# Kernel tuning notes

Hardware: AMD Instinct MI355X
Metric: run time of the kernel (lower is better)

Reference implementation:

```python
import jax, jax.numpy as jnp
import numpy as np

BATCH = 256
MAX_STEP = 200
NUM_Q = 1000


def setup_inputs() -> dict:
    key = jax.random.key(0)
    k1, k2 = jax.random.split(key)
    # predictions strictly inside (0, 1) for BCE
    pred = jax.random.uniform(k1, (BATCH, MAX_STEP - 1, NUM_Q), dtype=jnp.float32) * 0.98 + 0.01
    # sparse binary error-ID labels; some rows all-zero -> masked out (ragged structure)
    batch = (jax.random.uniform(k2, (BATCH, MAX_STEP, NUM_Q)) < 0.002).astype(jnp.float32)
    # guarantee every student has at least one attempted row (torch BCE on empty -> NaN)
    batch = batch.at[:, 1, 0].set(1.0)
    return {"pred": pred, "batch": batch}


def reference(pred, batch):
    # ErrorIDs path: gt = batch[student][1:], keep rows containing any 1.
    gt = batch[:, 1:, :]                              # [B, T-1, Q]
    row_mask = jnp.any(gt == 1.0, axis=-1)            # [B, T-1] ragged mask
    m = row_mask[:, :, None].astype(pred.dtype)       # [B, T-1, 1]

    # nn.BCELoss: -(y*log(p) + (1-y)*log(1-p)), logs clamped at -100, mean reduction
    log_p = jnp.maximum(jnp.log(pred), -100.0)
    log_1mp = jnp.maximum(jnp.log1p(-pred), -100.0)
    bce = -(gt * log_p + (1.0 - gt) * log_1mp)        # [B, T-1, Q]

    n_elem = row_mask.sum(axis=1).astype(pred.dtype) * gt.shape[-1]  # selected elements per student
    per_student = (bce * m).sum(axis=(1, 2)) / n_elem               # mean BCE per student
    loss = per_student.sum()                                        # summed over students

    # Original returns ragged concatenations of selected rows; we return the
    # equivalent masked full tensors plus the row mask (same information, jit-friendly).
    return (loss, pred * m, gt * m, row_mask)
```

## Files before the change

### kernel.cpp

```cpp
#include <hip/hip_runtime.h>

#define BATCHN 256
#define TSTEPS 199
#define NQ     1000
#define NROWS  (BATCHN * TSTEPS)
#define RPB    4
#define NBLOCKS (NROWS / RPB)

__global__ void zero_ws_kernel(float* __restrict__ ws) {
    int i = threadIdx.x;
    if (i < 2 * BATCHN) ws[i] = 0.0f;
}

typedef float f4v __attribute__((ext_vector_type(4)));

__device__ __forceinline__ f4v loadu4(const float* p) {
    f4v v; __builtin_memcpy(&v, p, 16); return v;
}

__global__ __launch_bounds__(256) void main_kernel(
    const float* __restrict__ pred,
    const float* __restrict__ batch,
    float* __restrict__ out,
    float* __restrict__ ws)
{
    const int wid  = threadIdx.x >> 6;
    const int lane = threadIdx.x & 63;
    const int r = blockIdx.x * RPB + wid;
    const int b = r / TSTEPS;
    const int t = r - b * TSTEPS;

    const float* prow = pred + (size_t)r * NQ;
    const float* grow = batch + ((size_t)b * 200 + t + 1) * NQ;

    const bool f3 = lane < 57;
    const int e = (lane == 57) ? 999 : (lane >= 58 && lane < 61) ? (lane - 58) : -1;

    const f4v z = {0.f, 0.f, 0.f, 0.f};

    f4v g0 = loadu4(grow + 3 + 4 * lane);
    f4v g1 = loadu4(grow + 3 + 4 * (lane + 64));
    f4v g2 = loadu4(grow + 3 + 4 * (lane + 128));
    f4v g3 = f3 ? loadu4(grow + 3 + 4 * (lane + 192)) : z;
    float gx = (e >= 0) ? grow[e] : 0.0f;

    f4v p0 = loadu4(prow + 3 + 4 * lane);
    f4v p1 = loadu4(prow + 3 + 4 * (lane + 64));
    f4v p2 = loadu4(prow + 3 + 4 * (lane + 128));
    f4v p3 = f3 ? loadu4(prow + 3 + 4 * (lane + 192)) : z;
    float px = (e >= 0) ? prow[e] : 0.0f;

    int any = (g0.x == 1.0f) | (g0.y == 1.0f) | (g0.z == 1.0f) | (g0.w == 1.0f)
            | (g1.x == 1.0f) | (g1.y == 1.0f) | (g1.z == 1.0f) | (g1.w == 1.0f)
            | (g2.x == 1.0f) | (g2.y == 1.0f) | (g2.z == 1.0f) | (g2.w == 1.0f)
            | (g3.x == 1.0f) | (g3.y == 1.0f) | (g3.z == 1.0f) | (g3.w == 1.0f)
            | (gx   == 1.0f);
    const unsigned long long bm = __ballot(any);
    const float m = bm ? 1.0f : 0.0f;

    float s = 0.0f;
    {
        const float pe[17] = {p0.x,p0.y,p0.z,p0.w, p1.x,p1.y,p1.z,p1.w,
                              p2.x,p2.y,p2.z,p2.w, p3.x,p3.y,p3.z,p3.w, px};
        const float ge[17] = {g0.x,g0.y,g0.z,g0.w, g1.x,g1.y,g1.z,g1.w,
                              g2.x,g2.y,g2.z,g2.w, g3.x,g3.y,g3.z,g3.w, gx};
        #pragma unroll
        for (int q = 0; q < 17; ++q) {
            const float lp = fmaxf(__logf(pe[q]),        -100.0f);
            const float l1 = fmaxf(__logf(1.0f - pe[q]), -100.0f);
            s -= l1 + ge[q] * (lp - l1);
        }
    }

    float* const orow_p   = out + 1 + (size_t)r * NQ;
    float* const orow_g   = out + 1 + (size_t)NROWS * NQ + (size_t)r * NQ;
    float* const out_mask = out + 1 + 2 * (size_t)NROWS * NQ;

    *(float4*)(orow_p + 3 + 4 * lane)         = make_float4(p0.x*m, p0.y*m, p0.z*m, p0.w*m);
    *(float4*)(orow_p + 3 + 4 * (lane + 64))  = make_float4(p1.x*m, p1.y*m, p1.z*m, p1.w*m);
    *(float4*)(orow_p + 3 + 4 * (lane + 128)) = make_float4(p2.x*m, p2.y*m, p2.z*m, p2.w*m);
    if (f3)
        *(float4*)(orow_p + 3 + 4 * (lane + 192)) = make_float4(p3.x*m, p3.y*m, p3.z*m, p3.w*m);

    *(float4*)(orow_g + 3 + 4 * lane)         = make_float4(g0.x*m, g0.y*m, g0.z*m, g0.w*m);
    *(float4*)(orow_g + 3 + 4 * (lane + 64))  = make_float4(g1.x*m, g1.y*m, g1.z*m, g1.w*m);
    *(float4*)(orow_g + 3 + 4 * (lane + 128)) = make_float4(g2.x*m, g2.y*m, g2.z*m, g2.w*m);
    if (f3)
        *(float4*)(orow_g + 3 + 4 * (lane + 192)) = make_float4(g3.x*m, g3.y*m, g3.z*m, g3.w*m);

    if (e >= 0) {
        orow_p[e] = px * m;
        orow_g[e] = gx * m;
    }

    #pragma unroll
    for (int off = 32; off > 0; off >>= 1) s += __shfl_down(s, off);

    if (lane == 0) {
        out_mask[r] = m;
        if (bm) {
            atomicAdd(&ws[b], s);
            atomicAdd(&ws[BATCHN + b], 1.0f);
        }
    }
}

__global__ __launch_bounds__(256) void final_kernel(
    float* __restrict__ out, const float* __restrict__ ws)
{
    const int b = threadIdx.x;
    float per = ws[b] / (ws[BATCHN + b] * (float)NQ);

    #pragma unroll
    for (int off = 32; off > 0; off >>= 1) per += __shfl_down(per, off);

    __shared__ float ssum[4];
    const int lane = b & 63, wid = b >> 6;
    if (lane == 0) ssum[wid] = per;
    __syncthreads();
    if (b == 0) out[0] = ssum[0] + ssum[1] + ssum[2] + ssum[3];
}

extern "C" void kernel_launch(void* const* d_in, const int* in_sizes, int n_in,
                              void* d_out, int out_size, void* d_ws, size_t ws_size,
                              hipStream_t stream) {
    const float* pred  = (const float*)d_in[0];
    const float* batch = (const float*)d_in[1];
    float* out = (float*)d_out;
    float* ws  = (float*)d_ws;

    zero_ws_kernel<<<1, 512, 0, stream>>>(ws);
    main_kernel<<<NBLOCKS, 256, 0, stream>>>(pred, batch, out, ws);
    final_kernel<<<1, 256, 0, stream>>>(out, ws);
}
```

Baseline: 700.1 us.

## Skip pred loads for masked rows and replace atomics with per-row partial sums

```diff
diff --git a/kernel.cpp b/kernel.cpp
--- a/kernel.cpp
+++ b/kernel.cpp
@@ -7,17 +7,18 @@
 #define RPB    4
 #define NBLOCKS (NROWS / RPB)
 
-__global__ void zero_ws_kernel(float* __restrict__ ws) {
-    int i = threadIdx.x;
-    if (i < 2 * BATCHN) ws[i] = 0.0f;
-}
-
 typedef float f4v __attribute__((ext_vector_type(4)));
 
 __device__ __forceinline__ f4v loadu4(const float* p) {
     f4v v; __builtin_memcpy(&v, p, 16); return v;
 }
 
+__global__ void zero_ws_kernel(float* __restrict__ ws) {
+    int i = threadIdx.x;
+    if (i < 2 * BATCHN) ws[i] = 0.0f;
+}
+
+template<bool ROWSUM>
 __global__ __launch_bounds__(256) void main_kernel(
     const float* __restrict__ pred,
     const float* __restrict__ batch,
@@ -35,7 +36,6 @@
 
     const bool f3 = lane < 57;
     const int e = (lane == 57) ? 999 : (lane >= 58 && lane < 61) ? (lane - 58) : -1;
-
     const f4v z = {0.f, 0.f, 0.f, 0.f};
 
     f4v g0 = loadu4(grow + 3 + 4 * lane);
@@ -44,19 +44,49 @@
     f4v g3 = f3 ? loadu4(grow + 3 + 4 * (lane + 192)) : z;
     float gx = (e >= 0) ? grow[e] : 0.0f;
 
+    int any = (g0.x == 1.0f) | (g0.y == 1.0f) | (g0.z == 1.0f) | (g0.w == 1.0f)
+            | (g1.x == 1.0f) | (g1.y == 1.0f) | (g1.z == 1.0f) | (g1.w == 1.0f)
+            | (g2.x == 1.0f) | (g2.y == 1.0f) | (g2.z == 1.0f) | (g2.w == 1.0f)
+            | (g3.x == 1.0f) | (g3.y == 1.0f) | (g3.z == 1.0f) | (g3.w == 1.0f)
+            | (gx   == 1.0f);
+    const unsigned long long bm = __ballot(any);
+
+    float* const orow_p   = out + 1 + (size_t)r * NQ;
+    float* const orow_g   = out + 1 + (size_t)NROWS * NQ + (size_t)r * NQ;
+    float* const out_mask = out + 1 + 2 * (size_t)NROWS * NQ;
+
+    if (!bm) {
+        *(f4v*)(orow_p + 3 + 4 * lane)         = z;
+        *(f4v*)(orow_p + 3 + 4 * (lane + 64))  = z;
+        *(f4v*)(orow_p + 3 + 4 * (lane + 128)) = z;
+        if (f3) *(f4v*)(orow_p + 3 + 4 * (lane + 192)) = z;
+        *(f4v*)(orow_g + 3 + 4 * lane)         = z;
+        *(f4v*)(orow_g + 3 + 4 * (lane + 64))  = z;
+        *(f4v*)(orow_g + 3 + 4 * (lane + 128)) = z;
+        if (f3) *(f4v*)(orow_g + 3 + 4 * (lane + 192)) = z;
+        if (e >= 0) { orow_p[e] = 0.0f; orow_g[e] = 0.0f; }
+        if (lane == 0) {
+            out_mask[r] = 0.0f;
+            if (ROWSUM) ws[r] = 0.0f;
+        }
+        return;
+    }
+
     f4v p0 = loadu4(prow + 3 + 4 * lane);
     f4v p1 = loadu4(prow + 3 + 4 * (lane + 64));
     f4v p2 = loadu4(prow + 3 + 4 * (lane + 128));
     f4v p3 = f3 ? loadu4(prow + 3 + 4 * (lane + 192)) : z;
     float px = (e >= 0) ? prow[e] : 0.0f;
 
-    int any = (g0.x == 1.0f) | (g0.y == 1.0f) | (g0.z == 1.0f) | (g0.w == 1.0f)
-            | (g1.x == 1.0f) | (g1.y == 1.0f) | (g1.z == 1.0f) | (g1.w == 1.0f)
-            | (g2.x == 1.0f) | (g2.y == 1.0f) | (g2.z == 1.0f) | (g2.w == 1.0f)
-            | (g3.x == 1.0f) | (g3.y == 1.0f) | (g3.z == 1.0f) | (g3.w == 1.0f)
-            | (gx   == 1.0f);
-    const unsigned long long bm = __ballot(any);
-    const float m = bm ? 1.0f : 0.0f;
+    *(f4v*)(orow_p + 3 + 4 * lane)         = p0;
+    *(f4v*)(orow_p + 3 + 4 * (lane + 64))  = p1;
+    *(f4v*)(orow_p + 3 + 4 * (lane + 128)) = p2;
+    if (f3) *(f4v*)(orow_p + 3 + 4 * (lane + 192)) = p3;
+    *(f4v*)(orow_g + 3 + 4 * lane)         = g0;
+    *(f4v*)(orow_g + 3 + 4 * (lane + 64))  = g1;
+    *(f4v*)(orow_g + 3 + 4 * (lane + 128)) = g2;
+    if (f3) *(f4v*)(orow_g + 3 + 4 * (lane + 192)) = g3;
+    if (e >= 0) { orow_p[e] = px; orow_g[e] = gx; }
 
     float s = 0.0f;
     {
@@ -72,37 +102,61 @@
         }
     }
 
-    float* const orow_p   = out + 1 + (size_t)r * NQ;
-    float* const orow_g   = out + 1 + (size_t)NROWS * NQ + (size_t)r * NQ;
-    float* const out_mask = out + 1 + 2 * (size_t)NROWS * NQ;
-
-    *(float4*)(orow_p + 3 + 4 * lane)         = make_float4(p0.x*m, p0.y*m, p0.z*m, p0.w*m);
-    *(float4*)(orow_p + 3 + 4 * (lane + 64))  = make_float4(p1.x*m, p1.y*m, p1.z*m, p1.w*m);
-    *(float4*)(orow_p + 3 + 4 * (lane + 128)) = make_float4(p2.x*m, p2.y*m, p2.z*m, p2.w*m);
-    if (f3)
-        *(float4*)(orow_p + 3 + 4 * (lane + 192)) = make_float4(p3.x*m, p3.y*m, p3.z*m, p3.w*m);
-
-    *(float4*)(orow_g + 3 + 4 * lane)         = make_float4(g0.x*m, g0.y*m, g0.z*m, g0.w*m);
-    *(float4*)(orow_g + 3 + 4 * (lane + 64))  = make_float4(g1.x*m, g1.y*m, g1.z*m, g1.w*m);
-    *(float4*)(orow_g + 3 + 4 * (lane + 128)) = make_float4(g2.x*m, g2.y*m, g2.z*m, g2.w*m);
-    if (f3)
-        *(float4*)(orow_g + 3 + 4 * (lane + 192)) = make_float4(g3.x*m, g3.y*m, g3.z*m, g3.w*m);
-
-    if (e >= 0) {
-        orow_p[e] = px * m;
-        orow_g[e] = gx * m;
-    }
-
     #pragma unroll
     for (int off = 32; off > 0; off >>= 1) s += __shfl_down(s, off);
 
     if (lane == 0) {
-        out_mask[r] = m;
-        if (bm) {
+        out_mask[r] = 1.0f;
+        if (ROWSUM) {
+            ws[r] = s;
+        } else {
             atomicAdd(&ws[b], s);
             atomicAdd(&ws[BATCHN + b], 1.0f);
         }
     }
+}
+
+__global__ __launch_bounds__(256) void reduce_kernel(
+    const float* __restrict__ out, float* __restrict__ ws)
+{
+    const int b = blockIdx.x;
+    const int i = threadIdx.x;
+    const float* out_mask = out + 1 + 2 * (size_t)NROWS * NQ;
+
+    float v = 0.0f, c = 0.0f;
+    if (i < TSTEPS) {
+        const int r = b * TSTEPS + i;
+        v = ws[r];
+        c = out_mask[r];
+    }
+    #pragma unroll
+    for (int off = 32; off > 0; off >>= 1) {
+        v += __shfl_down(v, off);
+        c += __shfl_down(c, off);
+    }
+    __shared__ float sv[4], sc[4];
+    const int lane = i & 63, w = i >> 6;
+    if (lane == 0) { sv[w] = v; sc[w] = c; }
+    __syncthreads();
+    if (i == 0) {
+        const float vt = sv[0] + sv[1] + sv[2] + sv[3];
+        const float ct = sc[0] + sc[1] + sc[2] + sc[3];
+        ws[NROWS + b] = vt / (ct * (float)NQ);
+    }
+}
+
+__global__ __launch_bounds__(256) void final2_kernel(
+    float* __restrict__ out, const float* __restrict__ ws)
+{
+    const int b = threadIdx.x;
+    float per = ws[NROWS + b];
+    #pragma unroll
+    for (int off = 32; off > 0; off >>= 1) per += __shfl_down(per, off);
+    __shared__ float ssum[4];
+    const int lane = b & 63, w = b >> 6;
+    if (lane == 0) ssum[w] = per;
+    __syncthreads();
+    if (b == 0) out[0] = ssum[0] + ssum[1] + ssum[2] + ssum[3];
 }
 
 __global__ __launch_bounds__(256) void final_kernel(
@@ -110,13 +164,11 @@
 {
     const int b = threadIdx.x;
     float per = ws[b] / (ws[BATCHN + b] * (float)NQ);
-
     #pragma unroll
     for (int off = 32; off > 0; off >>= 1) per += __shfl_down(per, off);
-
     __shared__ float ssum[4];
-    const int lane = b & 63, wid = b >> 6;
-    if (lane == 0) ssum[wid] = per;
+    const int lane = b & 63, w = b >> 6;
+    if (lane == 0) ssum[w] = per;
     __syncthreads();
     if (b == 0) out[0] = ssum[0] + ssum[1] + ssum[2] + ssum[3];
 }
@@ -129,7 +181,13 @@
     float* out = (float*)d_out;
     float* ws  = (float*)d_ws;
 
-    zero_ws_kernel<<<1, 512, 0, stream>>>(ws);
-    main_kernel<<<NBLOCKS, 256, 0, stream>>>(pred, batch, out, ws);
-    final_kernel<<<1, 256, 0, stream>>>(out, ws);
+    if (ws_size >= (size_t)(NROWS + BATCHN) * sizeof(float)) {
+        main_kernel<true><<<NBLOCKS, 256, 0, stream>>>(pred, batch, out, ws);
+        reduce_kernel<<<BATCHN, 256, 0, stream>>>(out, ws);
+        final2_kernel<<<1, 256, 0, stream>>>(out, ws);
+    } else {
+        zero_ws_kernel<<<1, 512, 0, stream>>>(ws);
+        main_kernel<false><<<NBLOCKS, 256, 0, stream>>>(pred, batch, out, ws);
+        final_kernel<<<1, 256, 0, stream>>>(out, ws);
+    }
 }
```

After: 649.7 us. -7.2%, faster.
